# Kernel tuning notes

Measured on AMD Instinct MI355X. Metric: run time of the kernel, lower is better.

The kernel has to match this reference:

```python
import jax, jax.numpy as jnp
import numpy as np
from jax import lax

B, T, D, H, L = 16, 256, 128, 128, 4  # batch, seq, input_size, hidden, num_layers
NUM_CLASSES = 10
EPS = 1e-5


def instancenorm(x):
    # x: [B, T, C]; InstanceNorm1d normalizes over the length dim (T) per (B, C),
    # biased variance, eps=1e-5, no affine.
    m = x.mean(axis=1, keepdims=True)
    v = x.var(axis=1, keepdims=True)
    return (x - m) / jnp.sqrt(v + EPS)


def lstm_stack(x, Wih, Whh, bih, bhh):
    # x: [B, T, I]; Wih/Whh: [L, 4H, I_or_H]; bih/bhh: [L, 4H]. Gate order i,f,g,o.
    batch = x.shape[0]
    hid = Whh.shape[-1]
    out = x
    for l in range(Wih.shape[0]):
        wih, whh, b = Wih[l], Whh[l], bih[l] + bhh[l]
        h0 = jnp.zeros((batch, hid), dtype=x.dtype)
        c0 = jnp.zeros((batch, hid), dtype=x.dtype)
        xs = out.swapaxes(0, 1)  # [T, B, I]

        def step(carry, xt):
            h, c = carry
            g = xt @ wih.T + h @ whh.T + b
            i, f, gg, o = jnp.split(g, 4, axis=-1)
            c_new = jax.nn.sigmoid(f) * c + jax.nn.sigmoid(i) * jnp.tanh(gg)
            h_new = jax.nn.sigmoid(o) * jnp.tanh(c_new)
            return (h_new, c_new), h_new

        _, hs = lax.scan(step, (h0, c0), xs)
        out = hs.swapaxes(0, 1)  # [B, T, H]
    return out


def setup_inputs() -> dict:
    key = jax.random.key(0)
    ks = jax.random.split(key, 16)
    s = 1.0 / np.sqrt(H)
    u = lambda k, shape: jax.random.uniform(k, shape, jnp.float32, -s, s)
    return {
        "x": jax.random.normal(ks[0], (B, T, D), jnp.float32),
        "Wih": u(ks[1], (L, 4 * H, D)),   # input_size == hidden_size so shapes stack
        "Whh": u(ks[2], (L, 4 * H, H)),
        "bih": u(ks[3], (L, 4 * H)),
        "bhh": u(ks[4], (L, 4 * H)),
        "proj_h_w": u(ks[5], (H, H)),
        "proj_h_b": u(ks[6], (H,)),
        "proj_x_w": u(ks[7], (H, D)),
        "proj_x_b": u(ks[8], (H,)),
        "attn_w": u(ks[9], (H,)),
        "fc_w": u(ks[10], (NUM_CLASSES, H)),
        "fc_b": u(ks[11], (NUM_CLASSES,)),
    }


def reference(x, Wih, Whh, bih, bhh, proj_h_w, proj_h_b, proj_x_w, proj_x_b, attn_w, fc_w, fc_b):
    batch, seq_len, input_dim = x.shape
    # normalize(): means/stdev are detached; torch std is unbiased (ddof=1)
    means = lax.stop_gradient(x.mean(axis=(0, 1), keepdims=True))
    stdev = lax.stop_gradient(x.std(axis=(0, 1), ddof=1, keepdims=True) + EPS)
    x = (x - means) / stdev
    x = instancenorm(x)

    lstm_out = lstm_stack(x, Wih, Whh, bih, bhh)   # dropout is identity in eval
    lstm_out = instancenorm(lstm_out)

    ph = lstm_out @ proj_h_w.T + proj_h_b           # [B, T, H]
    px = x @ proj_x_w.T + proj_x_b                  # [B, T, H]
    px = instancenorm(px)

    # additive attention over expanded [B, T, D, H] (values identical across D,
    # matching the original broadcast/expand semantics)
    combined = jnp.tanh(
        jnp.broadcast_to((ph + px)[:, :, None, :], (batch, seq_len, input_dim, ph.shape[-1]))
    )
    logits = jnp.einsum("btdh,h->btd", combined, attn_w)       # [B, T, D]
    alpha = jax.nn.softmax(logits.reshape(batch, -1), axis=1)   # softmax over T*D
    attention_map = alpha.reshape(batch, seq_len, input_dim)

    # classify: context = sum over (T, D) of lstm_out_ex * alpha
    context = jnp.einsum("bth,btd->bh", ph, attention_map)      # [B, H]
    out = context @ fc_w.T + fc_b                               # [B, num_classes]
    return out, attention_map
```

## Files before the change

### kernel.cpp

```cpp
#include <hip/hip_runtime.h>
#include <math.h>
#include <cstddef>

#define B_ 16
#define T_ 256
#define D_ 128
#define H_ 128
#define L_ 4
#define G_ 512
#define NC_ 10
#define EPS_ 1e-5f
#define C_ 16
#define NCHUNK_ (T_ / C_)

#define HROW_ 144
#define HOFF(k) ((k) + (((k) >> 5) << 2))

typedef float f4v __attribute__((ext_vector_type(4)));

#define LOAD_W8(w, base)                                                   \
    asm volatile(                                                          \
        "global_load_dwordx4 %0, %8, off\n\t"                             \
        "global_load_dwordx4 %1, %8, off offset:16\n\t"                   \
        "global_load_dwordx4 %2, %8, off offset:32\n\t"                   \
        "global_load_dwordx4 %3, %8, off offset:48\n\t"                   \
        "global_load_dwordx4 %4, %8, off offset:64\n\t"                   \
        "global_load_dwordx4 %5, %8, off offset:80\n\t"                   \
        "global_load_dwordx4 %6, %8, off offset:96\n\t"                   \
        "global_load_dwordx4 %7, %8, off offset:112\n\t"                  \
        "s_waitcnt vmcnt(0)"                                               \
        : "=&v"(w[0]), "=&v"(w[1]), "=&v"(w[2]), "=&v"(w[3]),              \
          "=&v"(w[4]), "=&v"(w[5]), "=&v"(w[6]), "=&v"(w[7])               \
        : "v"(base)                                                        \
        : "memory")

#define DOT32R(dst_, warr_, hvarr_)                                        \
    {                                                                      \
        float d0_ = 0.f, d1_ = 0.f;                                        \
        _Pragma("unroll")                                                  \
        for (int j_ = 0; j_ < 8; j_++) {                                   \
            d0_ = fmaf(warr_[j_].x, hvarr_[j_].x, d0_);                    \
            d1_ = fmaf(warr_[j_].y, hvarr_[j_].y, d1_);                    \
            d0_ = fmaf(warr_[j_].z, hvarr_[j_].z, d0_);                    \
            d1_ = fmaf(warr_[j_].w, hvarr_[j_].w, d1_);                    \
        }                                                                  \
        dst_ = d0_ + d1_;                                                  \
    }

#define LGKM_BAR_ asm volatile("s_waitcnt lgkmcnt(0)\n\ts_barrier" ::: "memory")

__device__ __forceinline__ float sigmoid_(float x) {
    x = fminf(fmaxf(x, -30.f), 30.f);
    return 1.f / (1.f + __expf(-x));
}
__device__ __forceinline__ float tanh_(float x) {
    float ax = fminf(fabsf(x), 15.f);
    float e = __expf(2.f * ax);
    float t = 1.f - 2.f / (e + 1.f);
    return copysignf(t, x);
}
__device__ __forceinline__ float qsum4_(float z) {
    int a = __builtin_amdgcn_update_dpp(0, __float_as_int(z), 0xB1, 0xF, 0xF, true);
    z += __int_as_float(a);
    int b = __builtin_amdgcn_update_dpp(0, __float_as_int(z), 0x4E, 0xF, 0xF, true);
    z += __int_as_float(b);
    return z;
}
__device__ __forceinline__ void wait_ge_(int* p, int v) {
    if (__hip_atomic_load(p, __ATOMIC_RELAXED, __HIP_MEMORY_SCOPE_AGENT) < v) {
        do { __builtin_amdgcn_s_sleep(1); }
        while (__hip_atomic_load(p, __ATOMIC_RELAXED, __HIP_MEMORY_SCOPE_AGENT) < v);
    }
    (void)__hip_atomic_load(p, __ATOMIC_ACQUIRE, __HIP_MEMORY_SCOPE_AGENT);
}
__device__ __forceinline__ void ast_(float* p, float v) {
    __hip_atomic_store(p, v, __ATOMIC_RELAXED, __HIP_MEMORY_SCOPE_AGENT);
}
__device__ __forceinline__ float ald_(const float* p) {
    return __hip_atomic_load(p, __ATOMIC_RELAXED, __HIP_MEMORY_SCOPE_AGENT);
}

#define REC_STEP(RD, WR, PI, PF, PG, PO)                                   \
    {                                                                      \
        const f4v* hb4_ = (const f4v*)(shbuf + (RD) * HROW_ + q * 36);     \
        f4v hv[8];                                                         \
        _Pragma("unroll")                                                  \
        for (int jj_ = 0; jj_ < 8; jj_++) hv[jj_] = hb4_[jj_];             \
        float zi, zf, zg, zo;                                              \
        DOT32R(zi, w0, hv);                                                \
        DOT32R(zf, w1, hv);                                                \
        DOT32R(zg, w2, hv);                                                \
        DOT32R(zo, w3, hv);                                                \
        zi = qsum4_(zi) + (PI); zf = qsum4_(zf) + (PF);                    \
        zg = qsum4_(zg) + (PG); zo = qsum4_(zo) + (PO);                    \
        float ai = sigmoid_(zi), af = sigmoid_(zf);                        \
        float ag = tanh_(zg),    ao = sigmoid_(zo);                        \
        c = fmaf(af, c, ai * ag);                                          \
        float hn = ao * tanh_(c);                                          \
        if (q == 0) {                                                      \
            shbuf[(WR) * HROW_ + HOFF(r)] = hn;                            \
            ast_(hst, hn);                                                 \
        }                                                                  \
        hst += 128;                                                        \
        LGKM_BAR_;                                                         \
    }

__global__ __attribute__((amdgpu_waves_per_eu(2, 2))) __launch_bounds__(512)
void megascan(const float* __restrict__ x,
              const float* __restrict__ Wih, const float* __restrict__ Whh,
              const float* __restrict__ bih, const float* __restrict__ bhh,
              const float* __restrict__ proj_x_w, const float* __restrict__ proj_x_b,
              const float* __restrict__ proj_h_w, const float* __restrict__ proj_h_b,
              const float* __restrict__ attn_w,
              const float* __restrict__ fc_w, const float* __restrict__ fc_b,
              float* __restrict__ mu_bd, float* __restrict__ invn,
              float* __restrict__ psumB, float* __restrict__ psqB,
              float* __restrict__ h_glob,
              float* __restrict__ ring,
              float* __restrict__ px,
              float* __restrict__ mu_px, float* __restrict__ inv_px,
              float* __restrict__ mu_ln, float* __restrict__ inv_ln,
              float* __restrict__ lsc,
              float* __restrict__ out, float* __restrict__ out_att,
              int* __restrict__ flag_h,
              int* __restrict__ flag_g,
              int* __restrict__ flag_px,
              int* __restrict__ flag_ln,
              int* __restrict__ cnt,
              int* __restrict__ flag_norm,
              int* __restrict__ cnt_s) {
    const int wg = blockIdx.x;
    const int tid = threadIdx.x;
    __shared__ __align__(16) float shbuf[16 * HROW_];
    __shared__ __align__(16) float sAs[64][32];
    __shared__ __align__(16) float sBs[32][132];
    __shared__ float sred[64][33];
    __shared__ float stmp[256], swsh[256], sctx[512];
    __shared__ float smu[128], siv[128];

    if (wg < 64) {
        const int r = tid >> 2, q = tid & 3;
        const int l = wg >> 4, b = wg & 15;
        f4v w0[8], w1[8], w2[8], w3[8];
        const float* wl = Whh + (size_t)l * G_ * 128;
        LOAD_W8(w0, wl + ((size_t)(0 * 128 + r)) * 128 + q * 32);
        LOAD_W8(w1, wl + ((size_t)(1 * 128 + r)) * 128 + q * 32);
        LOAD_W8(w2, wl + ((size_t)(2 * 128 + r)) * 128 + q * 32);
        LOAD_W8(w3, wl + ((size_t)(3 * 128 + r)) * 128 + q * 32);
        float c = 0.f;
        if (tid < HROW_) shbuf[tid] = 0.f;
        const float* rsl = ring + ((size_t)l * 16 + b) * (4 * C_ * G_);
        float* hob = h_glob + ((size_t)l * 16 + b) * T_ * 128;
        int* fg = flag_g + l * 16 + b;
        int* fh = flag_h + l * 16 + b;
        __syncthreads();

#pragma unroll 1
        for (int k = 0; k < NCHUNK_; k++) {
            if (tid == 0) wait_ge_(fg, k + 1);
            __syncthreads();
            const float* gb = rsl + (size_t)(k & 3) * C_ * G_;
            float* hst = hob + (size_t)k * C_ * 128 + r;
            float pc0 = ald_(gb + r),                pc1 = ald_(gb + 128 + r);
            float pc2 = ald_(gb + 256 + r),          pc3 = ald_(gb + 384 + r);
            float pc4 = ald_(gb + G_ + r),           pc5 = ald_(gb + G_ + 128 + r);
            float pc6 = ald_(gb + G_ + 256 + r),     pc7 = ald_(gb + G_ + 384 + r);
            float pn0 = ald_(gb + 2 * G_ + r),       pn1 = ald_(gb + 2 * G_ + 128 + r);
            float pn2 = ald_(gb + 2 * G_ + 256 + r), pn3 = ald_(gb + 2 * G_ + 384 + r);
            float pn4 = ald_(gb + 3 * G_ + r),       pn5 = ald_(gb + 3 * G_ + 128 + r);
            float pn6 = ald_(gb + 3 * G_ + 256 + r), pn7 = ald_(gb + 3 * G_ + 384 + r);
#pragma unroll 1
            for (int u = 0; u < 8; u++) {
                float nn0 = 0.f, nn1 = 0.f, nn2 = 0.f, nn3 = 0.f;
                float nn4 = 0.f, nn5 = 0.f, nn6 = 0.f, nn7 = 0.f;
                if (u < 6) {
                    const float* g2 = gb + (size_t)(2 * u + 4) * G_;
                    nn0 = ald_(g2 + r);            nn1 = ald_(g2 + 128 + r);
                    nn2 = ald_(g2 + 256 + r);      nn3 = ald_(g2 + 384 + r);
                    nn4 = ald_(g2 + G_ + r);       nn5 = ald_(g2 + G_ + 128 + r);
                    nn6 = ald_(g2 + G_ + 256 + r); nn7 = ald_(g2 + G_ + 384 + r);
                }
                REC_STEP(0, 1, pc0, pc1, pc2, pc3)
                REC_STEP(1, 0, pc4, pc5, pc6, pc7)
                pc0 = pn0; pc1 = pn1; pc2 = pn2; pc3 = pn3;
                pc4 = pn4; pc5 = pn5; pc6 = pn6; pc7 = pn7;
                pn0 = nn0; pn1 = nn1; pn2 = nn2; pn3 = nn3;
                pn4 = nn4; pn5 = nn5; pn6 = nn6; pn7 = nn7;
            }
            __syncthreads();
            if (tid == 0) __hip_atomic_store(fh, k + 1, __ATOMIC_RELEASE, __HIP_MEMORY_SCOPE_AGENT);
        }
    } else if (wg < 128) {
        const int r = tid >> 2, q = tid & 3;
        const int l = (wg - 64) >> 4, b = (wg - 64) & 15;
        f4v w0[8], w1[8], w2[8], w3[8];
        const float* wl = Wih + (size_t)l * G_ * 128;
        LOAD_W8(w0, wl + ((size_t)(0 * 128 + r)) * 128 + q * 32);
        LOAD_W8(w1, wl + ((size_t)(1 * 128 + r)) * 128 + q * 32);
        LOAD_W8(w2, wl + ((size_t)(2 * 128 + r)) * 128 + q * 32);
        LOAD_W8(w3, wl + ((size_t)(3 * 128 + r)) * 128 + q * 32);
        float bs0 = bih[l * G_ + r] + bhh[l * G_ + r];
        float bs1 = bih[l * G_ + 128 + r] + bhh[l * G_ + 128 + r];
        float bs2 = bih[l * G_ + 256 + r] + bhh[l * G_ + 256 + r];
        float bs3 = bih[l * G_ + 384 + r] + bhh[l * G_ + 384 + r];
        const float* hsrc = (l > 0) ? h_glob + ((size_t)(l - 1) * 16 + b) * T_ * 128
                                    : x + (size_t)b * T_ * 128;
        float muk = 0.f, ivk = 1.f;
        if (l == 0) {
            if (tid == 0) wait_ge_(flag_norm + b, 1);
            __syncthreads();
            muk = mu_bd[b * 128 + (tid & 127)];
            ivk = invn[b * 128 + (tid & 127)];
        }
        float* rout = ring + ((size_t)l * 16 + b) * (4 * C_ * G_);
        int* fhp = (l > 0) ? flag_h + (l - 1) * 16 + b : flag_h;
        int* fhme = flag_h + l * 16 + b;
        int* fgo = flag_g + l * 16 + b;

#pragma unroll 1
        for (int k = 0; k < NCHUNK_; k++) {
            if (tid == 0) {
                if (l > 0) wait_ge_(fhp, k + 1);
                if (k >= 4) wait_ge_(fhme, k - 3);
            }
            __syncthreads();
#pragma unroll
            for (int i = 0; i < 4; i++) {
                int idx = i * 512 + tid;
                float v;
                if (l == 0) {
                    v = hsrc[(size_t)k * C_ * 128 + idx];
                    v = (v - muk) * ivk;
                } else {
                    v = ald_(hsrc + (size_t)k * C_ * 128 + idx);
                }
                shbuf[(idx >> 7) * HROW_ + HOFF(idx & 127)] = v;
            }
            LGKM_BAR_;
#pragma unroll 4
            for (int s = 0; s < C_; s++) {
                const f4v* hb4 = (const f4v*)(shbuf + s * HROW_ + q * 36);
                f4v hv[8];
#pragma unroll
                for (int j = 0; j < 8; j++) hv[j] = hb4[j];
                float z0, z1, z2, z3;
                DOT32R(z0, w0, hv);
                DOT32R(z1, w1, hv);
                DOT32R(z2, w2, hv);
                DOT32R(z3, w3, hv);
                z0 = qsum4_(z0); z1 = qsum4_(z1);
                z2 = qsum4_(z2); z3 = qsum4_(z3);
                if (q == 0) {
                    float* ro = rout + ((size_t)(k & 3) * C_ + s) * G_;
                    ast_(ro + r, z0 + bs0);
                    ast_(ro + 128 + r, z1 + bs1);
                    ast_(ro + 256 + r, z2 + bs2);
                    ast_(ro + 384 + r, z3 + bs3);
                }
            }
            __syncthreads();
            if (tid == 0) __hip_atomic_store(fgo, k + 1, __ATOMIC_RELEASE, __HIP_MEMORY_SCOPE_AGENT);
        }
    } else if (wg < 144) {
        const int b = wg - 128;
        const int h = tid & 127, tq = tid >> 7;
        f4v w0[8], w1[8], w2[8], w3[8];
        LOAD_W8(w0, proj_x_w + (size_t)h * 128 + 0);
        LOAD_W8(w1, proj_x_w + (size_t)h * 128 + 32);
        LOAD_W8(w2, proj_x_w + (size_t)h * 128 + 64);
        LOAD_W8(w3, proj_x_w + (size_t)h * 128 + 96);
        float bsx = proj_x_b[h];
        if (tid == 0) wait_ge_(flag_norm + b, 1);
        __syncthreads();
        float muk = mu_bd[b * 128 + h], ivk = invn[b * 128 + h];
        const float* xb = x + (size_t)b * T_ * 128;
        float* pxb = px + (size_t)b * T_ * 128;
        float sacc = 0.f, qacc = 0.f;

        for (int blk = 0; blk < 16; blk++) {
            int t0 = blk * 16;
            __syncthreads();
#pragma unroll
            for (int j = 0; j < 4; j++) {
                int tt = tq * 4 + j;
                float v = xb[(size_t)(t0 + tt) * 128 + h];
                shbuf[tt * HROW_ + HOFF(h)] = (v - muk) * ivk;
            }
            __syncthreads();
#pragma unroll
            for (int j = 0; j < 4; j++) {
                int tt = tq * 4 + j;
                const float* row = shbuf + tt * HROW_;
                f4v hv[8];
                float p0, p1, p2, p3;
                const f4v* r4 = (const f4v*)(row + 0 * 36);
#pragma unroll
                for (int u = 0; u < 8; u++) hv[u] = r4[u];
                DOT32R(p0, w0, hv);
                r4 = (const f4v*)(row + 1 * 36);
#pragma unroll
                for (int u = 0; u < 8; u++) hv[u] = r4[u];
                DOT32R(p1, w1, hv);
                r4 = (const f4v*)(row + 2 * 36);
#pragma unroll
                for (int u = 0; u < 8; u++) hv[u] = r4[u];
                DOT32R(p2, w2, hv);
                r4 = (const f4v*)(row + 3 * 36);
#pragma unroll
                for (int u = 0; u < 8; u++) hv[u] = r4[u];
                DOT32R(p3, w3, hv);
                float val = (p0 + p1) + (p2 + p3) + bsx;
                ast_(pxb + (size_t)(t0 + tt) * 128 + h, val);
                sacc += val; qacc += val * val;
            }
        }
        __syncthreads();
        shbuf[tq * 128 + h] = sacc;
        shbuf[512 + tq * 128 + h] = qacc;
        __syncthreads();
        if (tq == 0) {
            float s = shbuf[h] + shbuf[128 + h] + shbuf[256 + h] + shbuf[384 + h];
            float qq = shbuf[512 + h] + shbuf[640 + h] + shbuf[768 + h] + shbuf[896 + h];
            float m = s * (1.f / T_);
            float v = qq * (1.f / T_) - m * m;
            ast_(mu_px + b * 128 + h, m);
            ast_(inv_px + b * 128 + h, rsqrtf(fmaxf(v, 0.f) + EPS_));
        }
        __syncthreads();
        if (tid == 0) __hip_atomic_store(flag_px + b, 1, __ATOMIC_RELEASE, __HIP_MEMORY_SCOPE_AGENT);
    } else if (wg < 160) {
        const int b = wg - 144;
        const int h = tid & 127, st = tid >> 7;
        const float* hsrc = h_glob + ((size_t)3 * 16 + b) * T_ * 128;
        int* f3 = flag_h + 3 * 16 + b;
        float s = 0.f, q = 0.f;
        for (int k = 0; k < NCHUNK_; k++) {
            if (tid == 0) wait_ge_(f3, k + 1);
            __syncthreads();
#pragma unroll
            for (int j = 0; j < 4; j++) {
                int tt = st * 4 + j;
                float v = ald_(hsrc + (size_t)(k * C_ + tt) * 128 + h);
                s += v; q += v * v;
            }
        }
        shbuf[st * 128 + h] = s;
        shbuf[512 + st * 128 + h] = q;
        __syncthreads();
        if (st == 0) {
            float ss = shbuf[h] + shbuf[128 + h] + shbuf[256 + h] + shbuf[384 + h];
            float qq = shbuf[512 + h] + shbuf[640 + h] + shbuf[768 + h] + shbuf[896 + h];
            float m = ss * (1.f / T_);
            float v = qq * (1.f / T_) - m * m;
            ast_(mu_ln + b * 128 + h, m);
            ast_(inv_ln + b * 128 + h, rsqrtf(fmaxf(v, 0.f) + EPS_));
        }
        __syncthreads();
        if (tid == 0) __hip_atomic_store(flag_ln + b, 1, __ATOMIC_RELEASE, __HIP_MEMORY_SCOPE_AGENT);
    } else if (wg < 224) {
        const int blk = wg - 160;
        const int b = blk >> 2, qt = blk & 3;
        const int m0 = qt * 64;
        if (tid == 0) { wait_ge_(flag_px + b, 1); wait_ge_(flag_ln + b, 1); }
        __syncthreads();
        if (tid < 128) {
            smu[tid] = mu_px[b * 128 + tid];
            siv[tid] = inv_px[b * 128 + tid];
        }
        __syncthreads();

        const float* h3b = h_glob + ((size_t)3 * 16 + b) * T_ * 128;
        float* phg = h_glob;
        const int lr = tid >> 3, lc = (tid & 7) << 2;
        const int nB = tid >> 2, k0B = (tid & 3) << 3;
        const int tm = (tid >> 5) << 2, tn = (tid & 31) << 2;
        float acc[4][4] = {};
        const float* mup = mu_ln + b * 128;
        const float* ivp = inv_ln + b * 128;
        for (int kb = 0; kb < 128; kb += 32) {
            float4 av = *(const float4*)(h3b + (size_t)(m0 + lr) * 128 + kb + lc);
            float4 m4 = *(const float4*)(mup + kb + lc);
            float4 i4 = *(const float4*)(ivp + kb + lc);
            av.x = (av.x - m4.x) * i4.x; av.y = (av.y - m4.y) * i4.y;
            av.z = (av.z - m4.z) * i4.z; av.w = (av.w - m4.w) * i4.w;
            float4 bv0 = *(const float4*)(proj_h_w + (size_t)nB * 128 + kb + k0B);
            float4 bv1 = *(const float4*)(proj_h_w + (size_t)nB * 128 + kb + k0B + 4);
            __syncthreads();
            *(float4*)&sAs[lr][lc] = av;
            sBs[k0B + 0][nB] = bv0.x; sBs[k0B + 1][nB] = bv0.y;
            sBs[k0B + 2][nB] = bv0.z; sBs[k0B + 3][nB] = bv0.w;
            sBs[k0B + 4][nB] = bv1.x; sBs[k0B + 5][nB] = bv1.y;
            sBs[k0B + 6][nB] = bv1.z; sBs[k0B + 7][nB] = bv1.w;
            __syncthreads();
#pragma unroll
            for (int k4 = 0; k4 < 8; k4++) {
                f4v a4[4];
#pragma unroll
                for (int i = 0; i < 4; i++) a4[i] = *(const f4v*)&sAs[tm + i][k4 * 4];
#pragma unroll
                for (int kk = 0; kk < 4; kk++) {
                    f4v b4 = *(const f4v*)&sBs[k4 * 4 + kk][tn];
#pragma unroll
                    for (int i = 0; i < 4; i++) {
                        acc[i][0] = fmaf(a4[i][kk], b4.x, acc[i][0]);
                        acc[i][1] = fmaf(a4[i][kk], b4.y, acc[i][1]);
                        acc[i][2] = fmaf(a4[i][kk], b4.z, acc[i][2]);
                        acc[i][3] = fmaf(a4[i][kk], b4.w, acc[i][3]);
                    }
                }
            }
        }
        float spart[4];
#pragma unroll
        for (int i = 0; i < 4; i++) {
            int t = m0 + tm + i;
            size_t prow = ((size_t)b * 256 + t) * 128;
            f4v pxv = *(const f4v*)(px + prow + tn);
            float sp = 0.f;
#pragma unroll
            for (int j = 0; j < 4; j++) {
                int col = tn + j;
                float val = acc[i][j] + proj_h_b[col];
                ast_(phg + prow + col, val);
                float inx = (pxv[j] - smu[col]) * siv[col];
                sp = fmaf(tanh_(val + inx), attn_w[col], sp);
            }
            spart[i] = sp;
        }
        __syncthreads();
#pragma unroll
        for (int i = 0; i < 4; i++) sred[tm + i][tid & 31] = spart[i];
        __syncthreads();
        if (tid < 64) {
            float s = 0.f;
#pragma unroll
            for (int j = 0; j < 32; j++) s += sred[tid][j];
            ast_(lsc + b * 256 + m0 + tid, s);
        }
        __syncthreads();
        if (tid == 0) {
            (void)__hip_atomic_fetch_add(cnt + b, 1, __ATOMIC_ACQ_REL, __HIP_MEMORY_SCOPE_AGENT);
            wait_ge_(cnt + b, 4);
        }
        __syncthreads();
        float v = 0.f;
        if (tid < 256) { v = lsc[b * 256 + tid]; stmp[tid] = v; }
        __syncthreads();
        for (int off = 128; off > 0; off >>= 1) {
            if (tid < off) stmp[tid] = fmaxf(stmp[tid], stmp[tid + off]);
            __syncthreads();
        }
        float mx = stmp[0];
        __syncthreads();
        float e = (tid < 256) ? __expf(v - mx) : 0.f;
        if (tid < 256) stmp[tid] = e;
        __syncthreads();
        for (int off = 128; off > 0; off >>= 1) {
            if (tid < off) stmp[tid] += stmp[tid + off];
            __syncthreads();
        }
        float tot = stmp[0];
        __syncthreads();
        if (tid < 256) swsh[tid] = e / tot;
        __syncthreads();
        {
            float* ob = out_att + (size_t)b * T_ * D_ + (size_t)m0 * 128;
            const float invD = 1.f / (float)D_;
            for (int i = tid; i < 64 * 128; i += 512)
                ob[i] = swsh[m0 + (i >> 7)] * invD;
        }
        if (qt == 0) {
            int h = tid & 127, st = tid >> 7;
            float a = 0.f;
            for (int tt = st * 64; tt < st * 64 + 64; tt++)
                a = fmaf(phg[((size_t)b * 256 + tt) * 128 + h], swsh[tt], a);
            sctx[st * 128 + h] = a;
            __syncthreads();
            if (tid < 128) sctx[tid] = sctx[tid] + sctx[128 + tid] + sctx[256 + tid] + sctx[384 + tid];
            __syncthreads();
            if (tid < NC_) {
                float s = fc_b[tid];
                const float* fw = fc_w + tid * 128;
                for (int k = 0; k < 128; k++) s = fmaf(sctx[k], fw[k], s);
                out[b * NC_ + tid] = s;
            }
        }
    } else {
        const int b = wg - 224;
        const int d = tid & 127, r = tid >> 7;
        const float* xb = x + (size_t)b * T_ * 128;
        float s = 0.f, q = 0.f;
        for (int t = r; t < T_; t += 4) {
            float v = xb[(size_t)t * 128 + d];
            s += v; q += v * v;
        }
        shbuf[tid] = s; shbuf[512 + tid] = q;
        __syncthreads();
        if (r == 0) {
            s = shbuf[d] + shbuf[128 + d] + shbuf[256 + d] + shbuf[384 + d];
            q = shbuf[512 + d] + shbuf[640 + d] + shbuf[768 + d] + shbuf[896 + d];
            ast_(psumB + b * 128 + d, s);
            ast_(psqB + b * 128 + d, q);
        }
        __syncthreads();
        if (tid == 0) {
            (void)__hip_atomic_fetch_add(cnt_s, 1, __ATOMIC_ACQ_REL, __HIP_MEMORY_SCOPE_AGENT);
            wait_ge_(cnt_s, 16);
        }
        __syncthreads();
        if (tid < 128) {
            float S = 0.f, Q = 0.f, sb = 0.f, qb = 0.f;
            for (int bb = 0; bb < 16; bb++) {
                float ps = psumB[bb * 128 + tid];
                float pq = psqB[bb * 128 + tid];
                S += ps; Q += pq;
                if (bb == b) { sb = ps; qb = pq; }
            }
            float n = (float)(B_ * T_);
            float m = S / n;
            float varu = (Q - n * m * m) / (n - 1.f);
            float sd = sqrtf(fmaxf(varu, 0.f)) + EPS_;
            float mu = sb * (1.f / T_);
            float varT = qb * (1.f / T_) - mu * mu;
            ast_(mu_bd + b * 128 + tid, mu);
            ast_(invn + b * 128 + tid, rsqrtf(fmaxf(varT, 0.f) + EPS_ * sd * sd));
        }
        __syncthreads();
        if (tid == 0) __hip_atomic_store(flag_norm + b, 1, __ATOMIC_RELEASE, __HIP_MEMORY_SCOPE_AGENT);
    }
}

extern "C" void kernel_launch(void* const* d_in, const int* in_sizes, int n_in,
                              void* d_out, int out_size, void* d_ws, size_t ws_size,
                              hipStream_t stream) {
    const float* x        = (const float*)d_in[0];
    const float* Wih      = (const float*)d_in[1];
    const float* Whh      = (const float*)d_in[2];
    const float* bih      = (const float*)d_in[3];
    const float* bhh      = (const float*)d_in[4];
    const float* proj_h_w = (const float*)d_in[5];
    const float* proj_h_b = (const float*)d_in[6];
    const float* proj_x_w = (const float*)d_in[7];
    const float* proj_x_b = (const float*)d_in[8];
    const float* attn_w   = (const float*)d_in[9];
    const float* fc_w     = (const float*)d_in[10];
    const float* fc_b     = (const float*)d_in[11];
    float* out = (float*)d_out;

    float* ws = (float*)d_ws;
    const size_t NTD = (size_t)B_ * T_ * D_;
    float* h_glob = ws;
    float* ring   = h_glob + 4 * NTD;
    float* px     = ring + 4 * NTD;
    float* smalls = px + NTD;
    float* psumB  = smalls;
    float* psqB   = psumB + 2048;
    float* mu_bd  = psqB + 2048;
    float* invn   = mu_bd + 2048;
    float* mu_ln  = invn + 2048;
    float* inv_ln = mu_ln + 2048;
    float* mu_px  = inv_ln + 2048;
    float* inv_px = mu_px + 2048;
    float* lsc    = inv_px + 2048;
    int*   flags  = (int*)(lsc + 4096);
    int*   flag_h   = flags;
    int*   flag_g   = flags + 64;
    int*   flag_px  = flags + 128;
    int*   flag_ln  = flags + 144;
    int*   cnt      = flags + 160;
    int*   flag_norm= flags + 176;
    int*   cnt_s    = flags + 192;

    hipMemsetAsync((void*)flags, 0, 256 * sizeof(int), stream);

    megascan<<<240, 512, 0, stream>>>(x, Wih, Whh, bih, bhh,
                                      proj_x_w, proj_x_b, proj_h_w, proj_h_b,
                                      attn_w, fc_w, fc_b,
                                      mu_bd, invn, psumB, psqB,
                                      h_glob, ring, px,
                                      mu_px, inv_px, mu_ln, inv_ln,
                                      lsc, out, out + B_ * NC_,
                                      flag_h, flag_g, flag_px, flag_ln, cnt,
                                      flag_norm, cnt_s);
}
```

Baseline: 455.4 us.

## Split LSTM gate dot products across 8 lanes with 1024-thread blocks

```diff
diff --git a/kernel.cpp b/kernel.cpp
--- a/kernel.cpp
+++ b/kernel.cpp
@@ -34,6 +34,17 @@
         : "v"(base)                                                        \
         : "memory")
 
+#define LOAD_W4(w, base)                                                   \
+    asm volatile(                                                          \
+        "global_load_dwordx4 %0, %4, off\n\t"                             \
+        "global_load_dwordx4 %1, %4, off offset:16\n\t"                   \
+        "global_load_dwordx4 %2, %4, off offset:32\n\t"                   \
+        "global_load_dwordx4 %3, %4, off offset:48\n\t"                   \
+        "s_waitcnt vmcnt(0)"                                               \
+        : "=&v"(w[0]), "=&v"(w[1]), "=&v"(w[2]), "=&v"(w[3])               \
+        : "v"(base)                                                        \
+        : "memory")
+
 #define DOT32R(dst_, warr_, hvarr_)                                        \
     {                                                                      \
         float d0_ = 0.f, d1_ = 0.f;                                        \
@@ -47,6 +58,19 @@
         dst_ = d0_ + d1_;                                                  \
     }
 
+#define DOT16R(dst_, warr_, hvarr_)                                        \
+    {                                                                      \
+        float d0_ = 0.f, d1_ = 0.f;                                        \
+        _Pragma("unroll")                                                  \
+        for (int j_ = 0; j_ < 4; j_++) {                                   \
+            d0_ = fmaf(warr_[j_].x, hvarr_[j_].x, d0_);                    \
+            d1_ = fmaf(warr_[j_].y, hvarr_[j_].y, d1_);                    \
+            d0_ = fmaf(warr_[j_].z, hvarr_[j_].z, d0_);                    \
+            d1_ = fmaf(warr_[j_].w, hvarr_[j_].w, d1_);                    \
+        }                                                                  \
+        dst_ = d0_ + d1_;                                                  \
+    }
+
 #define LGKM_BAR_ asm volatile("s_waitcnt lgkmcnt(0)\n\ts_barrier" ::: "memory")
 
 __device__ __forceinline__ float sigmoid_(float x) {
@@ -66,6 +90,11 @@
     z += __int_as_float(b);
     return z;
 }
+__device__ __forceinline__ float qsum8_(float z) {
+    z = qsum4_(z);
+    z += __shfl_xor(z, 4);
+    return z;
+}
 __device__ __forceinline__ void wait_ge_(int* p, int v) {
     if (__hip_atomic_load(p, __ATOMIC_RELAXED, __HIP_MEMORY_SCOPE_AGENT) < v) {
         do { __builtin_amdgcn_s_sleep(1); }
@@ -80,24 +109,32 @@
     return __hip_atomic_load(p, __ATOMIC_RELAXED, __HIP_MEMORY_SCOPE_AGENT);
 }
 
-#define REC_STEP(RD, WR, PI, PF, PG, PO)                                   \
+#define RING_LD8(dst_, gp_)                                                \
     {                                                                      \
-        const f4v* hb4_ = (const f4v*)(shbuf + (RD) * HROW_ + q * 36);     \
-        f4v hv[8];                                                         \
+        dst_[0] = ald_((gp_) + r);            dst_[1] = ald_((gp_) + 128 + r); \
+        dst_[2] = ald_((gp_) + 256 + r);      dst_[3] = ald_((gp_) + 384 + r); \
+        dst_[4] = ald_((gp_) + G_ + r);       dst_[5] = ald_((gp_) + G_ + 128 + r); \
+        dst_[6] = ald_((gp_) + G_ + 256 + r); dst_[7] = ald_((gp_) + G_ + 384 + r); \
+    }
+
+#define REC_STEP8(RD, WR, PI, PF, PG, PO)                                  \
+    {                                                                      \
+        const f4v* hb4_ = (const f4v*)(shbuf + (RD) * HROW_ + hq);         \
+        f4v hv[4];                                                         \
         _Pragma("unroll")                                                  \
-        for (int jj_ = 0; jj_ < 8; jj_++) hv[jj_] = hb4_[jj_];             \
+        for (int jj_ = 0; jj_ < 4; jj_++) hv[jj_] = hb4_[jj_];             \
         float zi, zf, zg, zo;                                              \
-        DOT32R(zi, w0, hv);                                                \
-        DOT32R(zf, w1, hv);                                                \
-        DOT32R(zg, w2, hv);                                                \
-        DOT32R(zo, w3, hv);                                                \
-        zi = qsum4_(zi) + (PI); zf = qsum4_(zf) + (PF);                    \
-        zg = qsum4_(zg) + (PG); zo = qsum4_(zo) + (PO);                    \
+        DOT16R(zi, w0, hv);                                                \
+        DOT16R(zf, w1, hv);                                                \
+        DOT16R(zg, w2, hv);                                                \
+        DOT16R(zo, w3, hv);                                                \
+        zi = qsum8_(zi) + (PI); zf = qsum8_(zf) + (PF);                    \
+        zg = qsum8_(zg) + (PG); zo = qsum8_(zo) + (PO);                    \
         float ai = sigmoid_(zi), af = sigmoid_(zf);                        \
         float ag = tanh_(zg),    ao = sigmoid_(zo);                        \
         c = fmaf(af, c, ai * ag);                                          \
         float hn = ao * tanh_(c);                                          \
-        if (q == 0) {                                                      \
+        if (qo == 0) {                                                     \
             shbuf[(WR) * HROW_ + HOFF(r)] = hn;                            \
             ast_(hst, hn);                                                 \
         }                                                                  \
@@ -105,7 +142,7 @@
         LGKM_BAR_;                                                         \
     }
 
-__global__ __attribute__((amdgpu_waves_per_eu(2, 2))) __launch_bounds__(512)
+__global__ __attribute__((amdgpu_waves_per_eu(4, 4))) __launch_bounds__(1024)
 void megascan(const float* __restrict__ x,
               const float* __restrict__ Wih, const float* __restrict__ Whh,
               const float* __restrict__ bih, const float* __restrict__ bhh,
@@ -139,14 +176,15 @@
     __shared__ float smu[128], siv[128];
 
     if (wg < 64) {
-        const int r = tid >> 2, q = tid & 3;
+        const int r = tid >> 3, qo = tid & 7;
+        const int hq = qo * 16 + ((qo >> 1) << 2);
         const int l = wg >> 4, b = wg & 15;
-        f4v w0[8], w1[8], w2[8], w3[8];
+        f4v w0[4], w1[4], w2[4], w3[4];
         const float* wl = Whh + (size_t)l * G_ * 128;
-        LOAD_W8(w0, wl + ((size_t)(0 * 128 + r)) * 128 + q * 32);
-        LOAD_W8(w1, wl + ((size_t)(1 * 128 + r)) * 128 + q * 32);
-        LOAD_W8(w2, wl + ((size_t)(2 * 128 + r)) * 128 + q * 32);
-        LOAD_W8(w3, wl + ((size_t)(3 * 128 + r)) * 128 + q * 32);
+        LOAD_W4(w0, wl + ((size_t)(0 * 128 + r)) * 128 + qo * 16);
+        LOAD_W4(w1, wl + ((size_t)(1 * 128 + r)) * 128 + qo * 16);
+        LOAD_W4(w2, wl + ((size_t)(2 * 128 + r)) * 128 + qo * 16);
+        LOAD_W4(w3, wl + ((size_t)(3 * 128 + r)) * 128 + qo * 16);
         float c = 0.f;
         if (tid < HROW_) shbuf[tid] = 0.f;
         const float* rsl = ring + ((size_t)l * 16 + b) * (4 * C_ * G_);
@@ -161,44 +199,36 @@
             __syncthreads();
             const float* gb = rsl + (size_t)(k & 3) * C_ * G_;
             float* hst = hob + (size_t)k * C_ * 128 + r;
-            float pc0 = ald_(gb + r),                pc1 = ald_(gb + 128 + r);
-            float pc2 = ald_(gb + 256 + r),          pc3 = ald_(gb + 384 + r);
-            float pc4 = ald_(gb + G_ + r),           pc5 = ald_(gb + G_ + 128 + r);
-            float pc6 = ald_(gb + G_ + 256 + r),     pc7 = ald_(gb + G_ + 384 + r);
-            float pn0 = ald_(gb + 2 * G_ + r),       pn1 = ald_(gb + 2 * G_ + 128 + r);
-            float pn2 = ald_(gb + 2 * G_ + 256 + r), pn3 = ald_(gb + 2 * G_ + 384 + r);
-            float pn4 = ald_(gb + 3 * G_ + r),       pn5 = ald_(gb + 3 * G_ + 128 + r);
-            float pn6 = ald_(gb + 3 * G_ + 256 + r), pn7 = ald_(gb + 3 * G_ + 384 + r);
+            float pc[8];
+            RING_LD8(pc, gb);
 #pragma unroll 1
             for (int u = 0; u < 8; u++) {
-                float nn0 = 0.f, nn1 = 0.f, nn2 = 0.f, nn3 = 0.f;
-                float nn4 = 0.f, nn5 = 0.f, nn6 = 0.f, nn7 = 0.f;
-                if (u < 6) {
-                    const float* g2 = gb + (size_t)(2 * u + 4) * G_;
-                    nn0 = ald_(g2 + r);            nn1 = ald_(g2 + 128 + r);
-                    nn2 = ald_(g2 + 256 + r);      nn3 = ald_(g2 + 384 + r);
-                    nn4 = ald_(g2 + G_ + r);       nn5 = ald_(g2 + G_ + 128 + r);
-                    nn6 = ald_(g2 + G_ + 256 + r); nn7 = ald_(g2 + G_ + 384 + r);
-                }
-                REC_STEP(0, 1, pc0, pc1, pc2, pc3)
-                REC_STEP(1, 0, pc4, pc5, pc6, pc7)
-                pc0 = pn0; pc1 = pn1; pc2 = pn2; pc3 = pn3;
-                pc4 = pn4; pc5 = pn5; pc6 = pn6; pc7 = pn7;
-                pn0 = nn0; pn1 = nn1; pn2 = nn2; pn3 = nn3;
-                pn4 = nn4; pn5 = nn5; pn6 = nn6; pn7 = nn7;
+                float pn[8];
+                if (u < 7) {
+                    const float* g2 = gb + (size_t)(2 * u + 2) * G_;
+                    RING_LD8(pn, g2);
+                } else {
+#pragma unroll
+                    for (int j = 0; j < 8; j++) pn[j] = 0.f;
+                }
+                REC_STEP8(0, 1, pc[0], pc[1], pc[2], pc[3])
+                REC_STEP8(1, 0, pc[4], pc[5], pc[6], pc[7])
+#pragma unroll
+                for (int j = 0; j < 8; j++) pc[j] = pn[j];
             }
             __syncthreads();
             if (tid == 0) __hip_atomic_store(fh, k + 1, __ATOMIC_RELEASE, __HIP_MEMORY_SCOPE_AGENT);
         }
     } else if (wg < 128) {
-        const int r = tid >> 2, q = tid & 3;
+        const int r = tid >> 3, qo = tid & 7;
+        const int hq = qo * 16 + ((qo >> 1) << 2);
         const int l = (wg - 64) >> 4, b = (wg - 64) & 15;
-        f4v w0[8], w1[8], w2[8], w3[8];
+        f4v w0[4], w1[4], w2[4], w3[4];
         const float* wl = Wih + (size_t)l * G_ * 128;
-        LOAD_W8(w0, wl + ((size_t)(0 * 128 + r)) * 128 + q * 32);
-        LOAD_W8(w1, wl + ((size_t)(1 * 128 + r)) * 128 + q * 32);
-        LOAD_W8(w2, wl + ((size_t)(2 * 128 + r)) * 128 + q * 32);
-        LOAD_W8(w3, wl + ((size_t)(3 * 128 + r)) * 128 + q * 32);
+        LOAD_W4(w0, wl + ((size_t)(0 * 128 + r)) * 128 + qo * 16);
+        LOAD_W4(w1, wl + ((size_t)(1 * 128 + r)) * 128 + qo * 16);
+        LOAD_W4(w2, wl + ((size_t)(2 * 128 + r)) * 128 + qo * 16);
+        LOAD_W4(w3, wl + ((size_t)(3 * 128 + r)) * 128 + qo * 16);
         float bs0 = bih[l * G_ + r] + bhh[l * G_ + r];
         float bs1 = bih[l * G_ + 128 + r] + bhh[l * G_ + 128 + r];
         float bs2 = bih[l * G_ + 256 + r] + bhh[l * G_ + 256 + r];
@@ -225,8 +255,8 @@
             }
             __syncthreads();
 #pragma unroll
-            for (int i = 0; i < 4; i++) {
-                int idx = i * 512 + tid;
+            for (int i = 0; i < 2; i++) {
+                int idx = i * 1024 + tid;
                 float v;
                 if (l == 0) {
                     v = hsrc[(size_t)k * C_ * 128 + idx];
@@ -239,18 +269,18 @@
             LGKM_BAR_;
 #pragma unroll 4
             for (int s = 0; s < C_; s++) {
-                const f4v* hb4 = (const f4v*)(shbuf + s * HROW_ + q * 36);
-                f4v hv[8];
-#pragma unroll
-                for (int j = 0; j < 8; j++) hv[j] = hb4[j];
+                const f4v* hb4 = (const f4v*)(shbuf + s * HROW_ + hq);
+                f4v hv[4];
+#pragma unroll
+                for (int j = 0; j < 4; j++) hv[j] = hb4[j];
                 float z0, z1, z2, z3;
-                DOT32R(z0, w0, hv);
-                DOT32R(z1, w1, hv);
-                DOT32R(z2, w2, hv);
-                DOT32R(z3, w3, hv);
-                z0 = qsum4_(z0); z1 = qsum4_(z1);
-                z2 = qsum4_(z2); z3 = qsum4_(z3);
-                if (q == 0) {
+                DOT16R(z0, w0, hv);
+                DOT16R(z1, w1, hv);
+                DOT16R(z2, w2, hv);
+                DOT16R(z3, w3, hv);
+                z0 = qsum8_(z0); z1 = qsum8_(z1);
+                z2 = qsum8_(z2); z3 = qsum8_(z3);
+                if (qo == 0) {
                     float* ro = rout + ((size_t)(k & 3) * C_ + s) * G_;
                     ast_(ro + r, z0 + bs0);
                     ast_(ro + 128 + r, z1 + bs1);
@@ -263,7 +293,8 @@
         }
     } else if (wg < 144) {
         const int b = wg - 128;
-        const int h = tid & 127, tq = tid >> 7;
+        const int h = tid & 127, tq = (tid >> 7) & 3;
+        const bool act = tid < 512;
         f4v w0[8], w1[8], w2[8], w3[8];
         LOAD_W8(w0, proj_x_w + (size_t)h * 128 + 0);
         LOAD_W8(w1, proj_x_w + (size_t)h * 128 + 32);
@@ -280,45 +311,51 @@
         for (int blk = 0; blk < 16; blk++) {
             int t0 = blk * 16;
             __syncthreads();
-#pragma unroll
-            for (int j = 0; j < 4; j++) {
-                int tt = tq * 4 + j;
-                float v = xb[(size_t)(t0 + tt) * 128 + h];
-                shbuf[tt * HROW_ + HOFF(h)] = (v - muk) * ivk;
-            }
-            __syncthreads();
-#pragma unroll
-            for (int j = 0; j < 4; j++) {
-                int tt = tq * 4 + j;
-                const float* row = shbuf + tt * HROW_;
-                f4v hv[8];
-                float p0, p1, p2, p3;
-                const f4v* r4 = (const f4v*)(row + 0 * 36);
-#pragma unroll
-                for (int u = 0; u < 8; u++) hv[u] = r4[u];
-                DOT32R(p0, w0, hv);
-                r4 = (const f4v*)(row + 1 * 36);
-#pragma unroll
-                for (int u = 0; u < 8; u++) hv[u] = r4[u];
-                DOT32R(p1, w1, hv);
-                r4 = (const f4v*)(row + 2 * 36);
-#pragma unroll
-                for (int u = 0; u < 8; u++) hv[u] = r4[u];
-                DOT32R(p2, w2, hv);
-                r4 = (const f4v*)(row + 3 * 36);
-#pragma unroll
-                for (int u = 0; u < 8; u++) hv[u] = r4[u];
-                DOT32R(p3, w3, hv);
-                float val = (p0 + p1) + (p2 + p3) + bsx;
-                ast_(pxb + (size_t)(t0 + tt) * 128 + h, val);
-                sacc += val; qacc += val * val;
-            }
-        }
-        __syncthreads();
-        shbuf[tq * 128 + h] = sacc;
-        shbuf[512 + tq * 128 + h] = qacc;
-        __syncthreads();
-        if (tq == 0) {
+            if (act) {
+#pragma unroll
+                for (int j = 0; j < 4; j++) {
+                    int tt = tq * 4 + j;
+                    float v = xb[(size_t)(t0 + tt) * 128 + h];
+                    shbuf[tt * HROW_ + HOFF(h)] = (v - muk) * ivk;
+                }
+            }
+            __syncthreads();
+            if (act) {
+#pragma unroll
+                for (int j = 0; j < 4; j++) {
+                    int tt = tq * 4 + j;
+                    const float* row = shbuf + tt * HROW_;
+                    f4v hv[8];
+                    float p0, p1, p2, p3;
+                    const f4v* r4 = (const f4v*)(row + 0 * 36);
+#pragma unroll
+                    for (int u = 0; u < 8; u++) hv[u] = r4[u];
+                    DOT32R(p0, w0, hv);
+                    r4 = (const f4v*)(row + 1 * 36);
+#pragma unroll
+                    for (int u = 0; u < 8; u++) hv[u] = r4[u];
+                    DOT32R(p1, w1, hv);
+                    r4 = (const f4v*)(row + 2 * 36);
+#pragma unroll
+                    for (int u = 0; u < 8; u++) hv[u] = r4[u];
+                    DOT32R(p2, w2, hv);
+                    r4 = (const f4v*)(row + 3 * 36);
+#pragma unroll
+                    for (int u = 0; u < 8; u++) hv[u] = r4[u];
+                    DOT32R(p3, w3, hv);
+                    float val = (p0 + p1) + (p2 + p3) + bsx;
+                    ast_(pxb + (size_t)(t0 + tt) * 128 + h, val);
+                    sacc += val; qacc += val * val;
+                }
+            }
+        }
+        __syncthreads();
+        if (act) {
+            shbuf[tq * 128 + h] = sacc;
+            shbuf[512 + tq * 128 + h] = qacc;
+        }
+        __syncthreads();
+        if (act && tq == 0) {
             float s = shbuf[h] + shbuf[128 + h] + shbuf[256 + h] + shbuf[384 + h];
             float qq = shbuf[512 + h] + shbuf[640 + h] + shbuf[768 + h] + shbuf[896 + h];
             float m = s * (1.f / T_);
@@ -330,24 +367,29 @@
         if (tid == 0) __hip_atomic_store(flag_px + b, 1, __ATOMIC_RELEASE, __HIP_MEMORY_SCOPE_AGENT);
     } else if (wg < 160) {
         const int b = wg - 144;
-        const int h = tid & 127, st = tid >> 7;
+        const int h = tid & 127, st = (tid >> 7) & 3;
+        const bool act = tid < 512;
         const float* hsrc = h_glob + ((size_t)3 * 16 + b) * T_ * 128;
         int* f3 = flag_h + 3 * 16 + b;
         float s = 0.f, q = 0.f;
         for (int k = 0; k < NCHUNK_; k++) {
             if (tid == 0) wait_ge_(f3, k + 1);
             __syncthreads();
-#pragma unroll
-            for (int j = 0; j < 4; j++) {
-                int tt = st * 4 + j;
-                float v = ald_(hsrc + (size_t)(k * C_ + tt) * 128 + h);
-                s += v; q += v * v;
-            }
-        }
-        shbuf[st * 128 + h] = s;
-        shbuf[512 + st * 128 + h] = q;
-        __syncthreads();
-        if (st == 0) {
+            if (act) {
+#pragma unroll
+                for (int j = 0; j < 4; j++) {
+                    int tt = st * 4 + j;
+                    float v = ald_(hsrc + (size_t)(k * C_ + tt) * 128 + h);
+                    s += v; q += v * v;
+                }
+            }
+        }
+        if (act) {
+            shbuf[st * 128 + h] = s;
+            shbuf[512 + st * 128 + h] = q;
+        }
+        __syncthreads();
+        if (act && st == 0) {
             float ss = shbuf[h] + shbuf[128 + h] + shbuf[256 + h] + shbuf[384 + h];
             float qq = shbuf[512 + h] + shbuf[640 + h] + shbuf[768 + h] + shbuf[896 + h];
             float m = ss * (1.f / T_);
@@ -361,6 +403,7 @@
         const int blk = wg - 160;
         const int b = blk >> 2, qt = blk & 3;
         const int m0 = qt * 64;
+        const bool act = tid < 512;
         if (tid == 0) { wait_ge_(flag_px + b, 1); wait_ge_(flag_ln + b, 1); }
         __syncthreads();
         if (tid < 128) {
@@ -373,63 +416,74 @@
         float* phg = h_glob;
         const int lr = tid >> 3, lc = (tid & 7) << 2;
         const int nB = tid >> 2, k0B = (tid & 3) << 3;
-        const int tm = (tid >> 5) << 2, tn = (tid & 31) << 2;
+        const int tm = ((tid >> 5) << 2) & 63, tn = (tid & 31) << 2;
         float acc[4][4] = {};
         const float* mup = mu_ln + b * 128;
         const float* ivp = inv_ln + b * 128;
         for (int kb = 0; kb < 128; kb += 32) {
-            float4 av = *(const float4*)(h3b + (size_t)(m0 + lr) * 128 + kb + lc);
-            float4 m4 = *(const float4*)(mup + kb + lc);
-            float4 i4 = *(const float4*)(ivp + kb + lc);
-            av.x = (av.x - m4.x) * i4.x; av.y = (av.y - m4.y) * i4.y;
-            av.z = (av.z - m4.z) * i4.z; av.w = (av.w - m4.w) * i4.w;
-            float4 bv0 = *(const float4*)(proj_h_w + (size_t)nB * 128 + kb + k0B);
-            float4 bv1 = *(const float4*)(proj_h_w + (size_t)nB * 128 + kb + k0B + 4);
-            __syncthreads();
-            *(float4*)&sAs[lr][lc] = av;
-            sBs[k0B + 0][nB] = bv0.x; sBs[k0B + 1][nB] = bv0.y;
-            sBs[k0B + 2][nB] = bv0.z; sBs[k0B + 3][nB] = bv0.w;
-            sBs[k0B + 4][nB] = bv1.x; sBs[k0B + 5][nB] = bv1.y;
-            sBs[k0B + 6][nB] = bv1.z; sBs[k0B + 7][nB] = bv1.w;
-            __syncthreads();
-#pragma unroll
-            for (int k4 = 0; k4 < 8; k4++) {
-                f4v a4[4];
-#pragma unroll
-                for (int i = 0; i < 4; i++) a4[i] = *(const f4v*)&sAs[tm + i][k4 * 4];
-#pragma unroll
-                for (int kk = 0; kk < 4; kk++) {
-                    f4v b4 = *(const f4v*)&sBs[k4 * 4 + kk][tn];
-#pragma unroll
-                    for (int i = 0; i < 4; i++) {
-                        acc[i][0] = fmaf(a4[i][kk], b4.x, acc[i][0]);
-                        acc[i][1] = fmaf(a4[i][kk], b4.y, acc[i][1]);
-                        acc[i][2] = fmaf(a4[i][kk], b4.z, acc[i][2]);
-                        acc[i][3] = fmaf(a4[i][kk], b4.w, acc[i][3]);
+            float4 av = {}, m4 = {}, i4 = {}, bv0 = {}, bv1 = {};
+            if (act) {
+                av = *(const float4*)(h3b + (size_t)(m0 + lr) * 128 + kb + lc);
+                m4 = *(const float4*)(mup + kb + lc);
+                i4 = *(const float4*)(ivp + kb + lc);
+                av.x = (av.x - m4.x) * i4.x; av.y = (av.y - m4.y) * i4.y;
+                av.z = (av.z - m4.z) * i4.z; av.w = (av.w - m4.w) * i4.w;
+                bv0 = *(const float4*)(proj_h_w + (size_t)nB * 128 + kb + k0B);
+                bv1 = *(const float4*)(proj_h_w + (size_t)nB * 128 + kb + k0B + 4);
+            }
+            __syncthreads();
+            if (act) {
+                *(float4*)&sAs[lr][lc] = av;
+                sBs[k0B + 0][nB] = bv0.x; sBs[k0B + 1][nB] = bv0.y;
+                sBs[k0B + 2][nB] = bv0.z; sBs[k0B + 3][nB] = bv0.w;
+                sBs[k0B + 4][nB] = bv1.x; sBs[k0B + 5][nB] = bv1.y;
+                sBs[k0B + 6][nB] = bv1.z; sBs[k0B + 7][nB] = bv1.w;
+            }
+            __syncthreads();
+            if (act) {
+#pragma unroll
+                for (int k4 = 0; k4 < 8; k4++) {
+                    f4v a4[4];
+#pragma unroll
+                    for (int i = 0; i < 4; i++) a4[i] = *(const f4v*)&sAs[tm + i][k4 * 4];
+#pragma unroll
+                    for (int kk = 0; kk < 4; kk++) {
+                        f4v b4 = *(const f4v*)&sBs[k4 * 4 + kk][tn];
+#pragma unroll
+                        for (int i = 0; i < 4; i++) {
+                            acc[i][0] = fmaf(a4[i][kk], b4.x, acc[i][0]);
+                            acc[i][1] = fmaf(a4[i][kk], b4.y, acc[i][1]);
+                            acc[i][2] = fmaf(a4[i][kk], b4.z, acc[i][2]);
+                            acc[i][3] = fmaf(a4[i][kk], b4.w, acc[i][3]);
+                        }
                     }
                 }
             }
         }
-        float spart[4];
-#pragma unroll
-        for (int i = 0; i < 4; i++) {
-            int t = m0 + tm + i;
-            size_t prow = ((size_t)b * 256 + t) * 128;
-            f4v pxv = *(const f4v*)(px + prow + tn);
-            float sp = 0.f;
-#pragma unroll
-            for (int j = 0; j < 4; j++) {
-                int col = tn + j;
-                float val = acc[i][j] + proj_h_b[col];
-                ast_(phg + prow + col, val);
-                float inx = (pxv[j] - smu[col]) * siv[col];
-                sp = fmaf(tanh_(val + inx), attn_w[col], sp);
-            }
-            spart[i] = sp;
-        }
-        __syncthreads();
-#pragma unroll
-        for (int i = 0; i < 4; i++) sred[tm + i][tid & 31] = spart[i];
+        float spart[4] = {};
+        if (act) {
+#pragma unroll
+            for (int i = 0; i < 4; i++) {
+                int t = m0 + tm + i;
+                size_t prow = ((size_t)b * 256 + t) * 128;
+                f4v pxv = *(const f4v*)(px + prow + tn);
+                float sp = 0.f;
+#pragma unroll
+                for (int j = 0; j < 4; j++) {
+                    int col = tn + j;
+                    float val = acc[i][j] + proj_h_b[col];
+                    ast_(phg + prow + col, val);
+                    float inx = (pxv[j] - smu[col]) * siv[col];
+                    sp = fmaf(tanh_(val + inx), attn_w[col], sp);
+                }
+                spart[i] = sp;
+            }
+        }
+        __syncthreads();
+        if (act) {
+#pragma unroll
+            for (int i = 0; i < 4; i++) sred[tm + i][tid & 31] = spart[i];
+        }
         __syncthreads();
         if (tid < 64) {
             float s = 0.f;
@@ -466,15 +520,17 @@
         {
             float* ob = out_att + (size_t)b * T_ * D_ + (size_t)m0 * 128;
             const float invD = 1.f / (float)D_;
-            for (int i = tid; i < 64 * 128; i += 512)
+            for (int i = tid; i < 64 * 128; i += 1024)
                 ob[i] = swsh[m0 + (i >> 7)] * invD;
         }
         if (qt == 0) {
-            int h = tid & 127, st = tid >> 7;
-            float a = 0.f;
-            for (int tt = st * 64; tt < st * 64 + 64; tt++)
-                a = fmaf(phg[((size_t)b * 256 + tt) * 128 + h], swsh[tt], a);
-            sctx[st * 128 + h] = a;
+            int hh = tid & 127, st = (tid >> 7) & 3;
+            if (act) {
+                float a = 0.f;
+                for (int tt = st * 64; tt < st * 64 + 64; tt++)
+                    a = fmaf(phg[((size_t)b * 256 + tt) * 128 + hh], swsh[tt], a);
+                sctx[st * 128 + hh] = a;
+            }
             __syncthreads();
             if (tid < 128) sctx[tid] = sctx[tid] + sctx[128 + tid] + sctx[256 + tid] + sctx[384 + tid];
             __syncthreads();
@@ -487,16 +543,19 @@
         }
     } else {
         const int b = wg - 224;
-        const int d = tid & 127, r = tid >> 7;
+        const int d = tid & 127, rr = (tid >> 7) & 3;
+        const bool act = tid < 512;
         const float* xb = x + (size_t)b * T_ * 128;
         float s = 0.f, q = 0.f;
-        for (int t = r; t < T_; t += 4) {
-            float v = xb[(size_t)t * 128 + d];
-            s += v; q += v * v;
-        }
-        shbuf[tid] = s; shbuf[512 + tid] = q;
-        __syncthreads();
-        if (r == 0) {
+        if (act) {
+            for (int t = rr; t < T_; t += 4) {
+                float v = xb[(size_t)t * 128 + d];
+                s += v; q += v * v;
+            }
+            shbuf[tid] = s; shbuf[512 + tid] = q;
+        }
+        __syncthreads();
+        if (act && rr == 0) {
             s = shbuf[d] + shbuf[128 + d] + shbuf[256 + d] + shbuf[384 + d];
             q = shbuf[512 + d] + shbuf[640 + d] + shbuf[768 + d] + shbuf[896 + d];
             ast_(psumB + b * 128 + d, s);
@@ -573,13 +632,13 @@
 
     hipMemsetAsync((void*)flags, 0, 256 * sizeof(int), stream);
 
-    megascan<<<240, 512, 0, stream>>>(x, Wih, Whh, bih, bhh,
-                                      proj_x_w, proj_x_b, proj_h_w, proj_h_b,
-                                      attn_w, fc_w, fc_b,
-                                      mu_bd, invn, psumB, psqB,
-                                      h_glob, ring, px,
-                                      mu_px, inv_px, mu_ln, inv_ln,
-                                      lsc, out, out + B_ * NC_,
-                                      flag_h, flag_g, flag_px, flag_ln, cnt,
-                                      flag_norm, cnt_s);
-}
+    megascan<<<240, 1024, 0, stream>>>(x, Wih, Whh, bih, bhh,
+                                       proj_x_w, proj_x_b, proj_h_w, proj_h_b,
+                                       attn_w, fc_w, fc_b,
+                                       mu_bd, invn, psumB, psqB,
+                                       h_glob, ring, px,
+                                       mu_px, inv_px, mu_ln, inv_ln,
+                                       lsc, out, out + B_ * NC_,
+                                       flag_h, flag_g, flag_px, flag_ln, cnt,
+                                       flag_norm, cnt_s);
+}
```

New measurement: 592.0 us. 1.3x slower.
